# Kernel tuning notes

Hardware: AMD Instinct MI355X
Metric: run time of the kernel (lower is better)

## Reference

```python
import jax, jax.numpy as jnp
import numpy as np


def setup_inputs() -> dict:
    key = jax.random.key(0)
    k1, k2 = jax.random.split(key)
    enc = jax.random.normal(k1, (32, 64, 64, 64), dtype=jnp.float32)   # (B, C, H, W), C == D
    embed = jax.random.normal(k2, (512, 64), dtype=jnp.float32)        # (K, D) codebook
    return {"enc": enc, "embed": embed}


def reference(enc, embed):
    B, C, H, W = enc.shape
    K, D = embed.shape
    # torch: enc.view(B, -1, C) with C == D -> plain reshape (no transpose), faithful to source.
    x = enc.reshape(B, -1, D)                                          # (B, N, D), N = C*H*W/D
    # Squared L2 distances; argmin is invariant under sqrt so we skip torch.cdist's sqrt.
    x_sq = jnp.sum(x * x, axis=-1, keepdims=True)                      # (B, N, 1)
    e_sq = jnp.sum(embed * embed, axis=-1)                             # (K,)
    d2 = x_sq - 2.0 * jnp.einsum('bnd,kd->bnk', x, embed) + e_sq       # (B, N, K)
    closest = jnp.argmin(d2, axis=-1)                                  # (B, N) int
    quantized = embed[closest]                                         # (B, N, D) gather
    commitment_loss = jnp.mean((jax.lax.stop_gradient(quantized) - x) ** 2)
    codebook_loss = jnp.mean((quantized - jax.lax.stop_gradient(x)) ** 2)
    quantize_loss = codebook_loss + 1.0 * commitment_loss
    # Straight-through estimator.
    quant_out = (x + jax.lax.stop_gradient(quantized - x)).reshape(B, C, H, W)
    return quant_out, quantize_loss, closest
```

## Files before the change

kernel.cpp:

```cpp
#include <hip/hip_runtime.h>
#include <math.h>

#define DQ 64
#define KQ 512
#define NVEC 131072
#define QOUT_SIZE (NVEC * DQ)
#define LOSS_OFF QOUT_SIZE
#define IDX_OFF (QOUT_SIZE + 1)

#define RPW 32
#define WPB 2
#define VPB (RPW * WPB)
#define NBLK (NVEC / VPB)
#define SC 64
#define NST (KQ / SC)
#define SDQ (SC * DQ)
#define TIE_THR 0.05f

typedef __attribute__((ext_vector_type(8))) _Float16 half8;
typedef __attribute__((ext_vector_type(4))) float f32x4;

static __device__ __forceinline__ void cvt8h(float4 a, float4 b, half8& h) {
    h[0] = (_Float16)a.x; h[1] = (_Float16)a.y; h[2] = (_Float16)a.z; h[3] = (_Float16)a.w;
    h[4] = (_Float16)b.x; h[5] = (_Float16)b.y; h[6] = (_Float16)b.z; h[7] = (_Float16)b.w;
}

__global__ void vq_init_kernel(const float* __restrict__ embed,
                               unsigned short* __restrict__ eh,
                               float* __restrict__ esq,
                               float* __restrict__ out) {
    const int t = blockIdx.x * 64 + threadIdx.x;
    if (t == 0) out[LOSS_OFF] = 0.0f;
    const int k = t >> 3;
    const int c = t & 7;
    const float4* p = (const float4*)(embed + (size_t)k * DQ + c * 8);
    float4 a = p[0], b = p[1];
    half8 h;
    cvt8h(a, b, h);
    const int slot = c ^ (k & 7);
    *(half8*)(eh + (size_t)k * DQ + slot * 8) = h;

    float ps = 0.f;
    ps = fmaf(a.x, a.x, ps); ps = fmaf(a.y, a.y, ps); ps = fmaf(a.z, a.z, ps); ps = fmaf(a.w, a.w, ps);
    ps = fmaf(b.x, b.x, ps); ps = fmaf(b.y, b.y, ps); ps = fmaf(b.z, b.z, ps); ps = fmaf(b.w, b.w, ps);
    ps += __shfl_xor(ps, 1);
    ps += __shfl_xor(ps, 2);
    ps += __shfl_xor(ps, 4);
    if (c == 0) esq[k] = ps;
}

__global__ __launch_bounds__(128) void vq_mfma_kernel(const float* __restrict__ enc,
                                                      const float* __restrict__ embed,
                                                      const unsigned short* __restrict__ eh,
                                                      const float* __restrict__ esq,
                                                      float* __restrict__ out) {
    __shared__ unsigned short hs[2 * SDQ];
    __shared__ float esq_s[KQ];
    __shared__ int bidx_s[VPB];
    __shared__ int flag_s[VPB];
    __shared__ float red[WPB];

    const int tid = threadIdx.x;
    const int lane = tid & 63;
    const int w = tid >> 6;
    const int l15 = lane & 15;
    const int l4 = lane >> 4;
    const int vb = blockIdx.x * VPB + w * RPW;

    esq_s[tid]       = esq[tid];
    esq_s[tid + 128] = esq[tid + 128];
    esq_s[tid + 256] = esq[tid + 256];
    esq_s[tid + 384] = esq[tid + 384];

    half8 ahA[2], ahB[2];
#pragma unroll
    for (int a = 0; a < 2; a++) {
        const float* base = enc + (size_t)(vb + a * 16 + l15) * DQ + l4 * 8;
        const float4* p0 = (const float4*)base;
        const float4* p1 = (const float4*)(base + 32);
        cvt8h(p0[0], p0[1], ahA[a]);
        cvt8h(p1[0], p1[1], ahB[a]);
    }

    float m1[8], m2[8];
    int i1[8];
#pragma unroll
    for (int r = 0; r < 8; r++) { m1[r] = 3.4e38f; m2[r] = 3.4e38f; i1[r] = 0; }

    const int sl0 = (l4 ^ (l15 & 7)) * 8;
    const int sl1 = sl0 ^ 32;

    half8 r0 = *(const half8*)(eh + tid * 8);
    half8 r1 = *(const half8*)(eh + 1024 + tid * 8);
    half8 r2 = *(const half8*)(eh + 2048 + tid * 8);
    half8 r3 = *(const half8*)(eh + 3072 + tid * 8);
    *(half8*)(hs + tid * 8) = r0;        *(half8*)(hs + 1024 + tid * 8) = r1;
    *(half8*)(hs + 2048 + tid * 8) = r2; *(half8*)(hs + 3072 + tid * 8) = r3;
    r0 = *(const half8*)(eh + SDQ + tid * 8);
    r1 = *(const half8*)(eh + SDQ + 1024 + tid * 8);
    r2 = *(const half8*)(eh + SDQ + 2048 + tid * 8);
    r3 = *(const half8*)(eh + SDQ + 3072 + tid * 8);

#define LDB(B0, B1, S) { const int _o = ((S) * 16 + l15) * DQ; \
    B0 = *(const half8*)(hb + _o + sl0); B1 = *(const half8*)(hb + _o + sl1); }

#define BODY(ST, S, B0, B1) { \
    const int code = (ST) * SC + (S) * 16 + l15; \
    const float ev = esq_s[code]; \
    _Pragma("unroll") \
    for (int a = 0; a < 2; a++) { \
        f32x4 acc = {0.f, 0.f, 0.f, 0.f}; \
        acc = __builtin_amdgcn_mfma_f32_16x16x32_f16(ahA[a], B0, acc, 0, 0, 0); \
        acc = __builtin_amdgcn_mfma_f32_16x16x32_f16(ahB[a], B1, acc, 0, 0, 0); \
        _Pragma("unroll") \
        for (int r = 0; r < 4; r++) { \
            float v = fmaf(-2.0f, acc[r], ev); \
            bool lt = v < m1[a * 4 + r]; \
            i1[a * 4 + r] = lt ? code : i1[a * 4 + r]; \
            m2[a * 4 + r] = fminf(m2[a * 4 + r], fmaxf(m1[a * 4 + r], v)); \
            m1[a * 4 + r] = fminf(m1[a * 4 + r], v); \
        } \
    } }

    for (int st = 0; st < NST; st++) {
        __syncthreads();
        if (st < NST - 1) {
            unsigned short* hw = hs + ((st + 1) & 1) * SDQ;
            *(half8*)(hw + tid * 8) = r0;        *(half8*)(hw + 1024 + tid * 8) = r1;
            *(half8*)(hw + 2048 + tid * 8) = r2; *(half8*)(hw + 3072 + tid * 8) = r3;
        }
        if (st < NST - 2) {
            const int o = (st + 2) * SDQ;
            r0 = *(const half8*)(eh + o + tid * 8);
            r1 = *(const half8*)(eh + o + 1024 + tid * 8);
            r2 = *(const half8*)(eh + o + 2048 + tid * 8);
            r3 = *(const half8*)(eh + o + 3072 + tid * 8);
        }
        const unsigned short* hb = hs + (st & 1) * SDQ;
        half8 b0h0, b0h1, b1h0, b1h1;
        LDB(b0h0, b0h1, 0)
        LDB(b1h0, b1h1, 1)
        BODY(st, 0, b0h0, b0h1)
        LDB(b0h0, b0h1, 2)
        BODY(st, 1, b1h0, b1h1)
        LDB(b1h0, b1h1, 3)
        BODY(st, 2, b0h0, b0h1)
        BODY(st, 3, b1h0, b1h1)
    }
#undef LDB
#undef BODY

#pragma unroll
    for (int m = 1; m <= 8; m <<= 1) {
#pragma unroll
        for (int r = 0; r < 8; r++) {
            float o1 = __shfl_xor(m1[r], m);
            float o2 = __shfl_xor(m2[r], m);
            int oi = __shfl_xor(i1[r], m);
            float nm2 = fminf(fminf(m2[r], o2), fmaxf(m1[r], o1));
            bool lt = o1 < m1[r];
            i1[r] = lt ? oi : i1[r];
            m1[r] = fminf(m1[r], o1);
            m2[r] = nm2;
        }
    }

    if (l15 == 0) {
#pragma unroll
        for (int a = 0; a < 2; a++)
#pragma unroll
            for (int r = 0; r < 4; r++) {
                const int row = a * 16 + l4 * 4 + r;
                bidx_s[w * RPW + row] = i1[a * 4 + r];
                flag_s[w * RPW + row] = (m2[a * 4 + r] - m1[a * 4 + r] < TIE_THR) ? 1 : 0;
            }
    }

    for (int row = 0; row < RPW; row++) {
        if (flag_s[w * RPW + row]) {
            const int v = vb + row;
            const float4* xe = (const float4*)(enc + (size_t)v * DQ);
            unsigned long long best = ~0ULL;
            for (int q = 0; q < 8; q++) {
                const int c = lane * 8 + q;
                const float4* ee = (const float4*)(embed + (size_t)c * DQ);
                double a = 0.0;
                for (int j = 0; j < 16; j++) {
                    float4 xx = xe[j], ez = ee[j];
                    double d0 = (double)xx.x - (double)ez.x; a = fma(d0, d0, a);
                    double d1 = (double)xx.y - (double)ez.y; a = fma(d1, d1, a);
                    double d2 = (double)xx.z - (double)ez.z; a = fma(d2, d2, a);
                    double d3 = (double)xx.w - (double)ez.w; a = fma(d3, d3, a);
                }
                unsigned long long p =
                    (((unsigned long long)__double_as_longlong(a)) & ~511ULL) | (unsigned)c;
                best = (p < best) ? p : best;
            }
#pragma unroll
            for (int mm = 1; mm < 64; mm <<= 1) {
                unsigned long long ob = (unsigned long long)__shfl_xor((long long)best, mm);
                best = (ob < best) ? ob : best;
            }
            if (lane == 0) bidx_s[w * RPW + row] = (int)(best & 511ULL);
        }
    }

    float lsum = 0.f;
#pragma unroll
    for (int a = 0; a < 2; a++) {
        const int myv = vb + a * 16 + l15;
        const int qb = bidx_s[w * RPW + a * 16 + l15];
        const float* qbase = embed + (size_t)qb * DQ + l4 * 8;
        const float4* qa = (const float4*)qbase;
        const float4* qc = (const float4*)(qbase + 32);
        float4 q0 = qa[0], q1 = qa[1], q2 = qc[0], q3 = qc[1];
        float* obase = out + (size_t)myv * DQ + l4 * 8;
        ((float4*)obase)[0] = q0; ((float4*)obase)[1] = q1;
        ((float4*)(obase + 32))[0] = q2; ((float4*)(obase + 32))[1] = q3;
        if (l4 == 0) out[IDX_OFF + myv] = (float)qb;

        float d;
        d = q0.x - (float)ahA[a][0]; lsum = fmaf(d, d, lsum);
        d = q0.y - (float)ahA[a][1]; lsum = fmaf(d, d, lsum);
        d = q0.z - (float)ahA[a][2]; lsum = fmaf(d, d, lsum);
        d = q0.w - (float)ahA[a][3]; lsum = fmaf(d, d, lsum);
        d = q1.x - (float)ahA[a][4]; lsum = fmaf(d, d, lsum);
        d = q1.y - (float)ahA[a][5]; lsum = fmaf(d, d, lsum);
        d = q1.z - (float)ahA[a][6]; lsum = fmaf(d, d, lsum);
        d = q1.w - (float)ahA[a][7]; lsum = fmaf(d, d, lsum);
        d = q2.x - (float)ahB[a][0]; lsum = fmaf(d, d, lsum);
        d = q2.y - (float)ahB[a][1]; lsum = fmaf(d, d, lsum);
        d = q2.z - (float)ahB[a][2]; lsum = fmaf(d, d, lsum);
        d = q2.w - (float)ahB[a][3]; lsum = fmaf(d, d, lsum);
        d = q3.x - (float)ahB[a][4]; lsum = fmaf(d, d, lsum);
        d = q3.y - (float)ahB[a][5]; lsum = fmaf(d, d, lsum);
        d = q3.z - (float)ahB[a][6]; lsum = fmaf(d, d, lsum);
        d = q3.w - (float)ahB[a][7]; lsum = fmaf(d, d, lsum);
    }

#pragma unroll
    for (int off = 32; off > 0; off >>= 1) lsum += __shfl_down(lsum, off);
    if (lane == 0) red[w] = lsum;
    __syncthreads();
    if (tid == 0) {
        float s = red[0] + red[1];
        atomicAdd(out + LOSS_OFF, s * (2.0f / (float)QOUT_SIZE));
    }
}

extern "C" void kernel_launch(void* const* d_in, const int* in_sizes, int n_in,
                              void* d_out, int out_size, void* d_ws, size_t ws_size,
                              hipStream_t stream) {
    const float* enc = (const float*)d_in[0];
    const float* embed = (const float*)d_in[1];
    float* out = (float*)d_out;
    unsigned short* eh = (unsigned short*)d_ws;
    float* esq = (float*)(eh + KQ * DQ);

    hipLaunchKernelGGL(vq_init_kernel, dim3(64), dim3(64), 0, stream,
                       embed, eh, esq, out);
    hipLaunchKernelGGL(vq_mfma_kernel, dim3(NBLK), dim3(128), 0, stream,
                       enc, embed, eh, esq, out);
}
```

Baseline: 162.9 us.

## Load whole fp16 codebook to LDS once and pack argmin index into float bits

Blocks grow from 2 to 8 waves, and each block stages the entire fp16 codebook (64 KB) into shared memory once, replacing the double-buffered streamed chunks and their per-stage barriers. The argmin index is now packed into the low 9 mantissa bits of the distance (with a positive offset added to esq so values stay positive), removing the separate index registers and index shuffles. Best and second-best tracking uses min plus med3. The packing costs distance precision, so the tie threshold is widened to send more rows to the exact fp64 fallback. The larger LDS footprint may lower blocks per CU.

```diff
diff --git a/kernel.cpp b/kernel.cpp
--- a/kernel.cpp
+++ b/kernel.cpp
@@ -9,13 +9,11 @@
 #define IDX_OFF (QOUT_SIZE + 1)
 
 #define RPW 32
-#define WPB 2
+#define WPB 8
 #define VPB (RPW * WPB)
 #define NBLK (NVEC / VPB)
-#define SC 64
-#define NST (KQ / SC)
-#define SDQ (SC * DQ)
-#define TIE_THR 0.05f
+#define ESQ_OFF 256.0f
+#define TIE_THR 0.09f
 
 typedef __attribute__((ext_vector_type(8))) _Float16 half8;
 typedef __attribute__((ext_vector_type(4))) float f32x4;
@@ -23,6 +21,10 @@
 static __device__ __forceinline__ void cvt8h(float4 a, float4 b, half8& h) {
     h[0] = (_Float16)a.x; h[1] = (_Float16)a.y; h[2] = (_Float16)a.z; h[3] = (_Float16)a.w;
     h[4] = (_Float16)b.x; h[5] = (_Float16)b.y; h[6] = (_Float16)b.z; h[7] = (_Float16)b.w;
+}
+
+static __device__ __forceinline__ float packk(float v, int code) {
+    return __uint_as_float((__float_as_uint(v) & 0xFFFFFE00u) | (unsigned)code);
 }
 
 __global__ void vq_init_kernel(const float* __restrict__ embed,
@@ -46,15 +48,15 @@
     ps += __shfl_xor(ps, 1);
     ps += __shfl_xor(ps, 2);
     ps += __shfl_xor(ps, 4);
-    if (c == 0) esq[k] = ps;
-}
-
-__global__ __launch_bounds__(128) void vq_mfma_kernel(const float* __restrict__ enc,
+    if (c == 0) esq[k] = ps + ESQ_OFF;
+}
+
+__global__ __launch_bounds__(512) void vq_mfma_kernel(const float* __restrict__ enc,
                                                       const float* __restrict__ embed,
                                                       const unsigned short* __restrict__ eh,
                                                       const float* __restrict__ esq,
                                                       float* __restrict__ out) {
-    __shared__ unsigned short hs[2 * SDQ];
+    __shared__ unsigned short hs[KQ * DQ];
     __shared__ float esq_s[KQ];
     __shared__ int bidx_s[VPB];
     __shared__ int flag_s[VPB];
@@ -67,10 +69,11 @@
     const int l4 = lane >> 4;
     const int vb = blockIdx.x * VPB + w * RPW;
 
-    esq_s[tid]       = esq[tid];
-    esq_s[tid + 128] = esq[tid + 128];
-    esq_s[tid + 256] = esq[tid + 256];
-    esq_s[tid + 384] = esq[tid + 384];
+#pragma unroll
+    for (int j = 0; j < 8; j++) {
+        *(half8*)(hs + j * 4096 + tid * 8) = *(const half8*)(eh + j * 4096 + tid * 8);
+    }
+    esq_s[tid] = esq[tid];
 
     half8 ahA[2], ahB[2];
 #pragma unroll
@@ -82,86 +85,55 @@
         cvt8h(p1[0], p1[1], ahB[a]);
     }
 
+    __syncthreads();
+
     float m1[8], m2[8];
-    int i1[8];
-#pragma unroll
-    for (int r = 0; r < 8; r++) { m1[r] = 3.4e38f; m2[r] = 3.4e38f; i1[r] = 0; }
+#pragma unroll
+    for (int r = 0; r < 8; r++) { m1[r] = 3.0e38f; m2[r] = 3.0e38f; }
 
     const int sl0 = (l4 ^ (l15 & 7)) * 8;
     const int sl1 = sl0 ^ 32;
-
-    half8 r0 = *(const half8*)(eh + tid * 8);
-    half8 r1 = *(const half8*)(eh + 1024 + tid * 8);
-    half8 r2 = *(const half8*)(eh + 2048 + tid * 8);
-    half8 r3 = *(const half8*)(eh + 3072 + tid * 8);
-    *(half8*)(hs + tid * 8) = r0;        *(half8*)(hs + 1024 + tid * 8) = r1;
-    *(half8*)(hs + 2048 + tid * 8) = r2; *(half8*)(hs + 3072 + tid * 8) = r3;
-    r0 = *(const half8*)(eh + SDQ + tid * 8);
-    r1 = *(const half8*)(eh + SDQ + 1024 + tid * 8);
-    r2 = *(const half8*)(eh + SDQ + 2048 + tid * 8);
-    r3 = *(const half8*)(eh + SDQ + 3072 + tid * 8);
-
-#define LDB(B0, B1, S) { const int _o = ((S) * 16 + l15) * DQ; \
-    B0 = *(const half8*)(hb + _o + sl0); B1 = *(const half8*)(hb + _o + sl1); }
-
-#define BODY(ST, S, B0, B1) { \
-    const int code = (ST) * SC + (S) * 16 + l15; \
-    const float ev = esq_s[code]; \
-    _Pragma("unroll") \
-    for (int a = 0; a < 2; a++) { \
-        f32x4 acc = {0.f, 0.f, 0.f, 0.f}; \
-        acc = __builtin_amdgcn_mfma_f32_16x16x32_f16(ahA[a], B0, acc, 0, 0, 0); \
-        acc = __builtin_amdgcn_mfma_f32_16x16x32_f16(ahB[a], B1, acc, 0, 0, 0); \
-        _Pragma("unroll") \
-        for (int r = 0; r < 4; r++) { \
-            float v = fmaf(-2.0f, acc[r], ev); \
-            bool lt = v < m1[a * 4 + r]; \
-            i1[a * 4 + r] = lt ? code : i1[a * 4 + r]; \
-            m2[a * 4 + r] = fminf(m2[a * 4 + r], fmaxf(m1[a * 4 + r], v)); \
-            m1[a * 4 + r] = fminf(m1[a * 4 + r], v); \
-        } \
-    } }
-
-    for (int st = 0; st < NST; st++) {
-        __syncthreads();
-        if (st < NST - 1) {
-            unsigned short* hw = hs + ((st + 1) & 1) * SDQ;
-            *(half8*)(hw + tid * 8) = r0;        *(half8*)(hw + 1024 + tid * 8) = r1;
-            *(half8*)(hw + 2048 + tid * 8) = r2; *(half8*)(hw + 3072 + tid * 8) = r3;
+    const unsigned short* hrow = hs + l15 * DQ;
+
+#pragma unroll 2
+    for (int p = 0; p < 16; p++) {
+        const int b0 = 2 * p, b1 = 2 * p + 1;
+        const half8 B00 = *(const half8*)(hrow + b0 * 1024 + sl0);
+        const half8 B01 = *(const half8*)(hrow + b0 * 1024 + sl1);
+        const half8 B10 = *(const half8*)(hrow + b1 * 1024 + sl0);
+        const half8 B11 = *(const half8*)(hrow + b1 * 1024 + sl1);
+        const float ev0 = esq_s[b0 * 16 + l15];
+        const float ev1 = esq_s[b1 * 16 + l15];
+        const int c0 = b0 * 16 + l15;
+        const int c1 = c0 + 16;
+#pragma unroll
+        for (int a = 0; a < 2; a++) {
+            f32x4 acc0 = {0.f, 0.f, 0.f, 0.f};
+            f32x4 acc1 = {0.f, 0.f, 0.f, 0.f};
+            acc0 = __builtin_amdgcn_mfma_f32_16x16x32_f16(ahA[a], B00, acc0, 0, 0, 0);
+            acc0 = __builtin_amdgcn_mfma_f32_16x16x32_f16(ahB[a], B01, acc0, 0, 0, 0);
+            acc1 = __builtin_amdgcn_mfma_f32_16x16x32_f16(ahA[a], B10, acc1, 0, 0, 0);
+            acc1 = __builtin_amdgcn_mfma_f32_16x16x32_f16(ahB[a], B11, acc1, 0, 0, 0);
+#pragma unroll
+            for (int r = 0; r < 4; r++) {
+                const int i = a * 4 + r;
+                const float k0 = packk(fmaf(-2.0f, acc0[r], ev0), c0);
+                const float k1 = packk(fmaf(-2.0f, acc1[r], ev1), c1);
+                const float mo = m1[i];
+                m1[i] = fminf(fminf(mo, k0), k1);
+                m2[i] = fminf(m2[i], __builtin_amdgcn_fmed3f(mo, k0, k1));
+            }
         }
-        if (st < NST - 2) {
-            const int o = (st + 2) * SDQ;
-            r0 = *(const half8*)(eh + o + tid * 8);
-            r1 = *(const half8*)(eh + o + 1024 + tid * 8);
-            r2 = *(const half8*)(eh + o + 2048 + tid * 8);
-            r3 = *(const half8*)(eh + o + 3072 + tid * 8);
-        }
-        const unsigned short* hb = hs + (st & 1) * SDQ;
-        half8 b0h0, b0h1, b1h0, b1h1;
-        LDB(b0h0, b0h1, 0)
-        LDB(b1h0, b1h1, 1)
-        BODY(st, 0, b0h0, b0h1)
-        LDB(b0h0, b0h1, 2)
-        BODY(st, 1, b1h0, b1h1)
-        LDB(b1h0, b1h1, 3)
-        BODY(st, 2, b0h0, b0h1)
-        BODY(st, 3, b1h0, b1h1)
-    }
-#undef LDB
-#undef BODY
+    }
 
 #pragma unroll
     for (int m = 1; m <= 8; m <<= 1) {
 #pragma unroll
         for (int r = 0; r < 8; r++) {
-            float o1 = __shfl_xor(m1[r], m);
-            float o2 = __shfl_xor(m2[r], m);
-            int oi = __shfl_xor(i1[r], m);
-            float nm2 = fminf(fminf(m2[r], o2), fmaxf(m1[r], o1));
-            bool lt = o1 < m1[r];
-            i1[r] = lt ? oi : i1[r];
+            const float o1 = __shfl_xor(m1[r], m);
+            const float o2 = __shfl_xor(m2[r], m);
+            m2[r] = fminf(fminf(m2[r], o2), fmaxf(m1[r], o1));
             m1[r] = fminf(m1[r], o1);
-            m2[r] = nm2;
         }
     }
 
@@ -171,7 +143,7 @@
 #pragma unroll
             for (int r = 0; r < 4; r++) {
                 const int row = a * 16 + l4 * 4 + r;
-                bidx_s[w * RPW + row] = i1[a * 4 + r];
+                bidx_s[w * RPW + row] = (int)(__float_as_uint(m1[a * 4 + r]) & 511u);
                 flag_s[w * RPW + row] = (m2[a * 4 + r] - m1[a * 4 + r] < TIE_THR) ? 1 : 0;
             }
     }
@@ -192,9 +164,9 @@
                     double d2 = (double)xx.z - (double)ez.z; a = fma(d2, d2, a);
                     double d3 = (double)xx.w - (double)ez.w; a = fma(d3, d3, a);
                 }
-                unsigned long long p =
+                unsigned long long pk =
                     (((unsigned long long)__double_as_longlong(a)) & ~511ULL) | (unsigned)c;
-                best = (p < best) ? p : best;
+                best = (pk < best) ? pk : best;
             }
 #pragma unroll
             for (int mm = 1; mm < 64; mm <<= 1) {
@@ -243,7 +215,8 @@
     if (lane == 0) red[w] = lsum;
     __syncthreads();
     if (tid == 0) {
-        float s = red[0] + red[1];
+        float s = ((red[0] + red[1]) + (red[2] + red[3]))
+                + ((red[4] + red[5]) + (red[6] + red[7]));
         atomicAdd(out + LOSS_OFF, s * (2.0f / (float)QOUT_SIZE));
     }
 }
@@ -259,6 +232,6 @@
 
     hipLaunchKernelGGL(vq_init_kernel, dim3(64), dim3(64), 0, stream,
                        embed, eh, esq, out);
-    hipLaunchKernelGGL(vq_mfma_kernel, dim3(NBLK), dim3(128), 0, stream,
+    hipLaunchKernelGGL(vq_mfma_kernel, dim3(NBLK), dim3(512), 0, stream,
                        enc, embed, eh, esq, out);
 }
```

After: 181.8 us. 1.12x slower.
